# Performance work log

Hardware: AMD Instinct MI355X
Metric: run time of the kernel (lower is better)

Reference implementation:

```python
import jax, jax.numpy as jnp
import numpy as np

N_NODES = 50000
N_EDGES = 800000
IN_CH, HID_CH, OUT_CH = 128, 256, 128


def setup_inputs() -> dict:
    key = jax.random.key(0)
    k1, k2, k3, k4 = jax.random.split(key, 4)
    x = jax.random.normal(k1, (N_NODES, IN_CH), dtype=jnp.float32)
    edge_index = jax.random.randint(k2, (2, N_EDGES), 0, N_NODES, dtype=jnp.int32)
    # Glorot-ish scaled weights
    W1 = jax.random.normal(k3, (IN_CH, HID_CH), dtype=jnp.float32) * (1.0 / np.sqrt(IN_CH))
    b1 = jnp.zeros((HID_CH,), dtype=jnp.float32)
    W2 = jax.random.normal(k4, (HID_CH, OUT_CH), dtype=jnp.float32) * (1.0 / np.sqrt(HID_CH))
    b2 = jnpp = jnp.zeros((OUT_CH,), dtype=jnp.float32)
    return {"x": x, "edge_index": edge_index, "W1": W1, "b1": b1, "W2": W2, "b2": b2}


def _gcn_conv(x, W, b, src, dst, num_nodes):
    """PyG GCNConv: add self-loops, symmetric deg^-1/2 norm, linear, scatter-add."""
    h = x @ W  # [N, out] dense transform first (as in GCNConv)
    # in-degree including self-loops (edge weights = 1)
    deg = jax.ops.segment_sum(jnp.ones_like(dst, dtype=h.dtype), dst, num_segments=num_nodes)
    deg = deg + 1.0  # self-loop contribution
    dinv = jnp.where(deg > 0, jax.lax.rsqrt(deg), 0.0)
    # neighbor messages: norm_e * h[src_e], scatter-added to dst
    norm = dinv[src] * dinv[dst]                      # [E]
    msg = h[src] * norm[:, None]                      # [E, out] gather
    agg = jax.ops.segment_sum(msg, dst, num_segments=num_nodes)  # scatter-add
    # self-loop messages: dinv[i]^2 * h[i]
    agg = agg + h * (dinv * dinv)[:, None]
    return agg + b


def reference(x, edge_index, W1, b1, W2, b2):
    src, dst = edge_index[0], edge_index[1]
    n = x.shape[0]
    h = jax.nn.relu(_gcn_conv(x, W1, b1, src, dst, n))
    return _gcn_conv(h, W2, b2, src, dst, n)
```

## Files before the change

### kernel.cpp

```cpp
#include <hip/hip_runtime.h>

#define N_NODES 50000
#define N_EDGES 800000
#define IN_CH 128
#define HID_CH 256
#define OUT_CH 128
#define BUCKET 64

#define N_XCD 8
#define NODES_PER_XCD 6250

using half8 = __attribute__((ext_vector_type(8))) _Float16;
using f32x4 = __attribute__((ext_vector_type(4))) float;


#define FILL_CHUNKS 3125
#define FILL_BLOCKS (FILL_CHUNKS * N_XCD)
#define CVT_BLOCKS 3125
#define WT1_BLOCKS 256
#define WT2_BLOCKS 128

__global__ __launch_bounds__(256) void prep_kernel(const int* __restrict__ src,
                                                   const int* __restrict__ dst,
                                                   int* __restrict__ cnt,
                                                   unsigned short* __restrict__ bucket,
                                                   const float* __restrict__ x,
                                                   _Float16* __restrict__ x16,
                                                   const float* __restrict__ W1,
                                                   _Float16* __restrict__ W1T,
                                                   const float* __restrict__ W2,
                                                   _Float16* __restrict__ W2T) {
    int b = blockIdx.x, t = threadIdx.x;
    if (b < FILL_BLOCKS) {
        int g = b & 7;
        int chunk = b >> 3;
        int i = chunk * 256 + t;
        if (i < N_EDGES) {
            int d = dst[i];
            int lo = g * NODES_PER_XCD;
            if (d >= lo && d < lo + NODES_PER_XCD) {
                int s = src[i];
                int p = atomicAdd(&cnt[d], 1);
                if (p < BUCKET) bucket[(size_t)d * BUCKET + p] = (unsigned short)s;
            }
        }
    } else if (b < FILL_BLOCKS + CVT_BLOCKS) {
        int i = (b - FILL_BLOCKS) * 256 + t;
        float4 v0 = ((const float4*)x)[i * 2];
        float4 v1 = ((const float4*)x)[i * 2 + 1];
        half8 o = {(_Float16)v0.x, (_Float16)v0.y, (_Float16)v0.z, (_Float16)v0.w,
                   (_Float16)v1.x, (_Float16)v1.y, (_Float16)v1.z, (_Float16)v1.w};
        ((half8*)x16)[i] = o;
    } else if (b < FILL_BLOCKS + CVT_BLOCKS + WT1_BLOCKS) {
        int n = b - FILL_BLOCKS - CVT_BLOCKS;
        if (t < IN_CH) W1T[(size_t)n * IN_CH + t] = (_Float16)W1[(size_t)t * HID_CH + n];
    } else {
        int n = b - FILL_BLOCKS - CVT_BLOCKS - WT1_BLOCKS;
        if (t < HID_CH) W2T[(size_t)n * HID_CH + t] = (_Float16)W2[(size_t)t * OUT_CH + n];
    }
}


template <bool OUT16>
__global__ __launch_bounds__(256) void agg16_kernel(const _Float16* __restrict__ h16,
                                                    const int* __restrict__ cnt,
                                                    const unsigned short* __restrict__ bucket,
                                                    const float* __restrict__ bias,
                                                    void* __restrict__ outp) {
    int t = blockIdx.x * 256 + threadIdx.x;
    int v = t >> 4;
    int sub = t & 15;
    int deg = min(cnt[v], BUCKET);
    float dv = rsqrtf((float)cnt[v] + 1.0f);
    half8 hv = ((const half8*)(h16 + (size_t)v * 128))[sub];
    float acc[8];
#pragma unroll
    for (int i = 0; i < 8; i++) acc[i] = (float)hv[i] * dv * dv;

    const unsigned short* bk = bucket + (size_t)v * BUCKET;
    for (int base = 0; base < deg; base += 16) {
        int idx = base + sub;
        int a = 0;
        float c = 0.f;
        if (idx < deg) {
            a = bk[idx];
            c = rsqrtf((float)cnt[a] + 1.0f) * dv;
        }
        int len = min(deg - base, 16);
        int j = 0;
        for (; j + 8 <= len; j += 8) {
            int   s0 = __shfl(a, j + 0, 16); float w0 = __shfl(c, j + 0, 16);
            int   s1 = __shfl(a, j + 1, 16); float w1 = __shfl(c, j + 1, 16);
            int   s2 = __shfl(a, j + 2, 16); float w2 = __shfl(c, j + 2, 16);
            int   s3 = __shfl(a, j + 3, 16); float w3 = __shfl(c, j + 3, 16);
            int   s4 = __shfl(a, j + 4, 16); float w4 = __shfl(c, j + 4, 16);
            int   s5 = __shfl(a, j + 5, 16); float w5 = __shfl(c, j + 5, 16);
            int   s6 = __shfl(a, j + 6, 16); float w6 = __shfl(c, j + 6, 16);
            int   s7 = __shfl(a, j + 7, 16); float w7 = __shfl(c, j + 7, 16);
            half8 x0 = ((const half8*)(h16 + (size_t)s0 * 128))[sub];
            half8 x1 = ((const half8*)(h16 + (size_t)s1 * 128))[sub];
            half8 x2 = ((const half8*)(h16 + (size_t)s2 * 128))[sub];
            half8 x3 = ((const half8*)(h16 + (size_t)s3 * 128))[sub];
            half8 x4 = ((const half8*)(h16 + (size_t)s4 * 128))[sub];
            half8 x5 = ((const half8*)(h16 + (size_t)s5 * 128))[sub];
            half8 x6 = ((const half8*)(h16 + (size_t)s6 * 128))[sub];
            half8 x7 = ((const half8*)(h16 + (size_t)s7 * 128))[sub];
#pragma unroll
            for (int i = 0; i < 8; i++) acc[i] += w0 * (float)x0[i];
#pragma unroll
            for (int i = 0; i < 8; i++) acc[i] += w1 * (float)x1[i];
#pragma unroll
            for (int i = 0; i < 8; i++) acc[i] += w2 * (float)x2[i];
#pragma unroll
            for (int i = 0; i < 8; i++) acc[i] += w3 * (float)x3[i];
#pragma unroll
            for (int i = 0; i < 8; i++) acc[i] += w4 * (float)x4[i];
#pragma unroll
            for (int i = 0; i < 8; i++) acc[i] += w5 * (float)x5[i];
#pragma unroll
            for (int i = 0; i < 8; i++) acc[i] += w6 * (float)x6[i];
#pragma unroll
            for (int i = 0; i < 8; i++) acc[i] += w7 * (float)x7[i];
        }
        for (; j + 4 <= len; j += 4) {
            int   s0 = __shfl(a, j + 0, 16); float w0 = __shfl(c, j + 0, 16);
            int   s1 = __shfl(a, j + 1, 16); float w1 = __shfl(c, j + 1, 16);
            int   s2 = __shfl(a, j + 2, 16); float w2 = __shfl(c, j + 2, 16);
            int   s3 = __shfl(a, j + 3, 16); float w3 = __shfl(c, j + 3, 16);
            half8 x0 = ((const half8*)(h16 + (size_t)s0 * 128))[sub];
            half8 x1 = ((const half8*)(h16 + (size_t)s1 * 128))[sub];
            half8 x2 = ((const half8*)(h16 + (size_t)s2 * 128))[sub];
            half8 x3 = ((const half8*)(h16 + (size_t)s3 * 128))[sub];
#pragma unroll
            for (int i = 0; i < 8; i++) acc[i] += w0 * (float)x0[i];
#pragma unroll
            for (int i = 0; i < 8; i++) acc[i] += w1 * (float)x1[i];
#pragma unroll
            for (int i = 0; i < 8; i++) acc[i] += w2 * (float)x2[i];
#pragma unroll
            for (int i = 0; i < 8; i++) acc[i] += w3 * (float)x3[i];
        }
        for (; j < len; j++) {
            int   s = __shfl(a, j, 16);
            float w = __shfl(c, j, 16);
            half8 xv = ((const half8*)(h16 + (size_t)s * 128))[sub];
#pragma unroll
            for (int i = 0; i < 8; i++) acc[i] += w * (float)xv[i];
        }
    }

    if (OUT16) {
        half8 o;
#pragma unroll
        for (int i = 0; i < 8; i++) o[i] = (_Float16)acc[i];
        ((half8*)outp)[(size_t)v * 16 + sub] = o;
    } else {
        const float4* bp = (const float4*)bias;
        float4 b0 = bp[sub * 2], b1v = bp[sub * 2 + 1];
        float4 o0 = make_float4(acc[0] + b0.x, acc[1] + b0.y, acc[2] + b0.z, acc[3] + b0.w);
        float4 o1 = make_float4(acc[4] + b1v.x, acc[5] + b1v.y, acc[6] + b1v.z, acc[7] + b1v.w);
        float4* op = (float4*)outp;
        op[(size_t)v * 32 + sub * 2] = o0;
        op[(size_t)v * 32 + sub * 2 + 1] = o1;
    }
}


__global__ __launch_bounds__(256) void fused_mlp_kernel(const _Float16* __restrict__ A,
                                                        const _Float16* __restrict__ W1T,
                                                        const float* __restrict__ b1,
                                                        const _Float16* __restrict__ W2T,
                                                        _Float16* __restrict__ T2, int M) {
    const int LDH = 264;
    const int LDA = 136;
    const int LDB = 40;
    __shared__ __align__(16) _Float16 h1s[64 * LDH];
    __shared__ __align__(16) _Float16 As[64 * LDA];
    __shared__ __align__(16) _Float16 Bs[128 * LDB];

    int tid = threadIdx.x;
    int wave = tid >> 6, lane = tid & 63;
    int quad = lane >> 4, l16 = lane & 15;
    int wm = wave >> 1, wn = wave & 1;
    int bm = blockIdx.x * 64;

    for (int q = tid; q < 64 * 16; q += 256) {
        int row = q >> 4, seg = q & 15;
        int gr = bm + row;
        float4 v = make_float4(0.f, 0.f, 0.f, 0.f);
        if (gr < M) v = *(const float4*)(A + (size_t)gr * IN_CH + seg * 8);
        *(float4*)(As + row * LDA + seg * 8) = v;
    }

    for (int nh = 0; nh < 2; nh++) {
        f32x4 acc[2][4] = {};
        for (int k0 = 0; k0 < IN_CH; k0 += 32) {
            for (int q = tid; q < 512; q += 256) {
                int row = q >> 2, seg = q & 3;
                float4 v = *(const float4*)(W1T + (size_t)(nh * 128 + row) * IN_CH + k0 + seg * 8);
                *(float4*)(Bs + row * LDB + seg * 8) = v;
            }
            __syncthreads();
            half8 af[2], bf[4];
#pragma unroll
            for (int mt = 0; mt < 2; mt++)
                af[mt] = *(const half8*)(As + (wm * 32 + mt * 16 + l16) * LDA + k0 + quad * 8);
#pragma unroll
            for (int nt = 0; nt < 4; nt++)
                bf[nt] = *(const half8*)(Bs + (wn * 64 + nt * 16 + l16) * LDB + quad * 8);
#pragma unroll
            for (int mt = 0; mt < 2; mt++)
#pragma unroll
                for (int nt = 0; nt < 4; nt++)
                    acc[mt][nt] = __builtin_amdgcn_mfma_f32_16x16x32_f16(af[mt], bf[nt], acc[mt][nt], 0, 0, 0);
            __syncthreads();
        }
#pragma unroll
        for (int mt = 0; mt < 2; mt++)
#pragma unroll
            for (int nt = 0; nt < 4; nt++)
#pragma unroll
                for (int r = 0; r < 4; r++) {
                    int ml = wm * 32 + mt * 16 + quad * 4 + r;
                    int nl = wn * 64 + nt * 16 + l16;
                    float v = acc[mt][nt][r] + b1[nh * 128 + nl];
                    h1s[ml * LDH + nh * 128 + nl] = (_Float16)fmaxf(v, 0.f);
                }
    }

    f32x4 acc2[2][4] = {};
    for (int k0 = 0; k0 < HID_CH; k0 += 32) {
        for (int q = tid; q < 512; q += 256) {
            int row = q >> 2, seg = q & 3;
            float4 v = *(const float4*)(W2T + (size_t)row * HID_CH + k0 + seg * 8);
            *(float4*)(Bs + row * LDB + seg * 8) = v;
        }
        __syncthreads();
        half8 af[2], bf[4];
#pragma unroll
        for (int mt = 0; mt < 2; mt++)
            af[mt] = *(const half8*)(h1s + (wm * 32 + mt * 16 + l16) * LDH + k0 + quad * 8);
#pragma unroll
        for (int nt = 0; nt < 4; nt++)
            bf[nt] = *(const half8*)(Bs + (wn * 64 + nt * 16 + l16) * LDB + quad * 8);
#pragma unroll
        for (int mt = 0; mt < 2; mt++)
#pragma unroll
            for (int nt = 0; nt < 4; nt++)
                acc2[mt][nt] = __builtin_amdgcn_mfma_f32_16x16x32_f16(af[mt], bf[nt], acc2[mt][nt], 0, 0, 0);
        __syncthreads();
    }

    _Float16* Cs = As;
#pragma unroll
    for (int mt = 0; mt < 2; mt++)
#pragma unroll
        for (int nt = 0; nt < 4; nt++)
#pragma unroll
            for (int r = 0; r < 4; r++) {
                int ml = wm * 32 + mt * 16 + quad * 4 + r;
                int nl = wn * 64 + nt * 16 + l16;
                Cs[ml * LDA + nl] = (_Float16)acc2[mt][nt][r];
            }
    __syncthreads();
    for (int q = tid; q < 64 * 16; q += 256) {
        int row = q >> 4, seg = q & 15;
        int gr = bm + row;
        if (gr < M)
            *(float4*)(T2 + (size_t)gr * OUT_CH + seg * 8) = *(const float4*)(Cs + row * LDA + seg * 8);
    }
}


extern "C" void kernel_launch(void* const* d_in, const int* in_sizes, int n_in,
                              void* d_out, int out_size, void* d_ws, size_t ws_size,
                              hipStream_t stream) {
    const float* x  = (const float*)d_in[0];
    const int*   ei = (const int*)d_in[1];
    const int*   src = ei;
    const int*   dst = ei + N_EDGES;
    const float* W1 = (const float*)d_in[2];
    const float* b1 = (const float*)d_in[3];
    const float* W2 = (const float*)d_in[4];
    const float* b2 = (const float*)d_in[5];
    float* out = (float*)d_out;

    char* w = (char*)d_ws;
    auto alloc = [&](size_t bytes) -> void* {
        void* p = (void*)w;
        w += (bytes + 255) & ~(size_t)255;
        return p;
    };
    int*            cnt    = (int*)alloc((size_t)N_NODES * 4);
    unsigned short* bucket = (unsigned short*)alloc((size_t)N_NODES * BUCKET * 2);
    _Float16*       x16    = (_Float16*)alloc((size_t)N_NODES * IN_CH * 2);
    _Float16*       a1     = (_Float16*)alloc((size_t)N_NODES * IN_CH * 2);
    _Float16*       t2     = (_Float16*)alloc((size_t)N_NODES * OUT_CH * 2);
    _Float16*       W1T    = (_Float16*)alloc((size_t)IN_CH * HID_CH * 2);
    _Float16*       W2T    = (_Float16*)alloc((size_t)HID_CH * OUT_CH * 2);

    hipMemsetAsync(cnt, 0, (size_t)N_NODES * 4, stream);

    prep_kernel<<<FILL_BLOCKS + CVT_BLOCKS + WT1_BLOCKS + WT2_BLOCKS, 256, 0, stream>>>(
        src, dst, cnt, bucket, x, x16, W1, W1T, W2, W2T);

    agg16_kernel<true><<<N_NODES * 16 / 256, 256, 0, stream>>>(x16, cnt, bucket, nullptr, a1);
    fused_mlp_kernel<<<(N_NODES + 63) / 64, 256, 0, stream>>>(a1, W1T, b1, W2T, t2, N_NODES);
    agg16_kernel<false><<<N_NODES * 16 / 256, 256, 0, stream>>>(t2, cnt, bucket, b2, out);
}
```

Baseline: 216.2 us.

## Replace global-atomic CSR fill with two-pass LDS binning by destination block

Edge bucketing becomes two passes. The first kernel builds a per-block LDS histogram over 128-node bins, reserves space with one global atomic per bin, and writes packed (src, local dst) entries into bin buffers. A second kernel per bin counts and fills per-node buckets with LDS atomics and writes cnt directly. This removes the 8x redundant scan of the edge list and the per-edge global atomics on cnt, at the cost of an extra launch and a fixed bin capacity that can drop edges if a bin overflows.

```diff
diff --git a/kernel.cpp b/kernel.cpp
--- a/kernel.cpp
+++ b/kernel.cpp
@@ -7,57 +7,100 @@
 #define OUT_CH 128
 #define BUCKET 64
 
-#define N_XCD 8
-#define NODES_PER_XCD 6250
-
 using half8 = __attribute__((ext_vector_type(8))) _Float16;
 using f32x4 = __attribute__((ext_vector_type(4))) float;
 
 
-#define FILL_CHUNKS 3125
-#define FILL_BLOCKS (FILL_CHUNKS * N_XCD)
+#define NB 391
+#define NPB 128
+#define BIN_CAP 2432
+#define A_CHUNK 2048
+#define A_BLOCKS 391
+
 #define CVT_BLOCKS 3125
 #define WT1_BLOCKS 256
 #define WT2_BLOCKS 128
 
-__global__ __launch_bounds__(256) void prep_kernel(const int* __restrict__ src,
-                                                   const int* __restrict__ dst,
-                                                   int* __restrict__ cnt,
-                                                   unsigned short* __restrict__ bucket,
-                                                   const float* __restrict__ x,
-                                                   _Float16* __restrict__ x16,
-                                                   const float* __restrict__ W1,
-                                                   _Float16* __restrict__ W1T,
-                                                   const float* __restrict__ W2,
-                                                   _Float16* __restrict__ W2T) {
+__global__ __launch_bounds__(256) void prepA_kernel(const int* __restrict__ src,
+                                                    const int* __restrict__ dst,
+                                                    int* __restrict__ bin_fill,
+                                                    unsigned int* __restrict__ binbuf,
+                                                    const float* __restrict__ x,
+                                                    _Float16* __restrict__ x16,
+                                                    const float* __restrict__ W1,
+                                                    _Float16* __restrict__ W1T,
+                                                    const float* __restrict__ W2,
+                                                    _Float16* __restrict__ W2T) {
+    __shared__ int hist[NB];
+    __shared__ int lbase[NB];
+    __shared__ int cur[NB];
     int b = blockIdx.x, t = threadIdx.x;
-    if (b < FILL_BLOCKS) {
-        int g = b & 7;
-        int chunk = b >> 3;
-        int i = chunk * 256 + t;
-        if (i < N_EDGES) {
-            int d = dst[i];
-            int lo = g * NODES_PER_XCD;
-            if (d >= lo && d < lo + NODES_PER_XCD) {
+    if (b < A_BLOCKS) {
+        for (int i = t; i < NB; i += 256) {
+            hist[i] = 0;
+            cur[i] = 0;
+        }
+        __syncthreads();
+        int e0 = b * A_CHUNK;
+        int d[8];
+#pragma unroll
+        for (int k = 0; k < 8; k++) {
+            int i = e0 + k * 256 + t;
+            d[k] = (i < N_EDGES) ? dst[i] : -1;
+            if (d[k] >= 0) atomicAdd(&hist[d[k] >> 7], 1);
+        }
+        __syncthreads();
+        for (int i = t; i < NB; i += 256)
+            if (hist[i]) lbase[i] = atomicAdd(&bin_fill[i], hist[i]);
+        __syncthreads();
+#pragma unroll
+        for (int k = 0; k < 8; k++) {
+            int i = e0 + k * 256 + t;
+            if (d[k] >= 0) {
+                int bin = d[k] >> 7;
                 int s = src[i];
-                int p = atomicAdd(&cnt[d], 1);
-                if (p < BUCKET) bucket[(size_t)d * BUCKET + p] = (unsigned short)s;
+                int o = atomicAdd(&cur[bin], 1);
+                int pos = lbase[bin] + o;
+                if (pos < BIN_CAP)
+                    binbuf[(size_t)bin * BIN_CAP + pos] =
+                        (unsigned)s | ((unsigned)(d[k] & (NPB - 1)) << 16);
             }
         }
-    } else if (b < FILL_BLOCKS + CVT_BLOCKS) {
-        int i = (b - FILL_BLOCKS) * 256 + t;
+    } else if (b < A_BLOCKS + CVT_BLOCKS) {
+        int i = (b - A_BLOCKS) * 256 + t;
         float4 v0 = ((const float4*)x)[i * 2];
         float4 v1 = ((const float4*)x)[i * 2 + 1];
         half8 o = {(_Float16)v0.x, (_Float16)v0.y, (_Float16)v0.z, (_Float16)v0.w,
                    (_Float16)v1.x, (_Float16)v1.y, (_Float16)v1.z, (_Float16)v1.w};
         ((half8*)x16)[i] = o;
-    } else if (b < FILL_BLOCKS + CVT_BLOCKS + WT1_BLOCKS) {
-        int n = b - FILL_BLOCKS - CVT_BLOCKS;
+    } else if (b < A_BLOCKS + CVT_BLOCKS + WT1_BLOCKS) {
+        int n = b - A_BLOCKS - CVT_BLOCKS;
         if (t < IN_CH) W1T[(size_t)n * IN_CH + t] = (_Float16)W1[(size_t)t * HID_CH + n];
     } else {
-        int n = b - FILL_BLOCKS - CVT_BLOCKS - WT1_BLOCKS;
+        int n = b - A_BLOCKS - CVT_BLOCKS - WT1_BLOCKS;
         if (t < HID_CH) W2T[(size_t)n * HID_CH + t] = (_Float16)W2[(size_t)t * OUT_CH + n];
     }
+}
+
+__global__ __launch_bounds__(256) void prepB_kernel(const int* __restrict__ bin_fill,
+                                                    const unsigned int* __restrict__ binbuf,
+                                                    int* __restrict__ cnt,
+                                                    unsigned short* __restrict__ bucket) {
+    __shared__ int lcnt[NPB];
+    int bin = blockIdx.x, t = threadIdx.x;
+    if (t < NPB) lcnt[t] = 0;
+    __syncthreads();
+    int n = min(bin_fill[bin], BIN_CAP);
+    for (int i = t; i < n; i += 256) {
+        unsigned e = binbuf[(size_t)bin * BIN_CAP + i];
+        int dl = e >> 16;
+        int s = e & 0xFFFF;
+        int p = atomicAdd(&lcnt[dl], 1);
+        if (p < BUCKET) bucket[((size_t)(bin * NPB + dl)) * BUCKET + p] = (unsigned short)s;
+    }
+    __syncthreads();
+    int v = bin * NPB + t;
+    if (t < NPB && v < N_NODES) cnt[v] = lcnt[t];
 }
 
 
@@ -291,18 +334,21 @@
         w += (bytes + 255) & ~(size_t)255;
         return p;
     };
-    int*            cnt    = (int*)alloc((size_t)N_NODES * 4);
-    unsigned short* bucket = (unsigned short*)alloc((size_t)N_NODES * BUCKET * 2);
-    _Float16*       x16    = (_Float16*)alloc((size_t)N_NODES * IN_CH * 2);
-    _Float16*       a1     = (_Float16*)alloc((size_t)N_NODES * IN_CH * 2);
-    _Float16*       t2     = (_Float16*)alloc((size_t)N_NODES * OUT_CH * 2);
-    _Float16*       W1T    = (_Float16*)alloc((size_t)IN_CH * HID_CH * 2);
-    _Float16*       W2T    = (_Float16*)alloc((size_t)HID_CH * OUT_CH * 2);
-
-    hipMemsetAsync(cnt, 0, (size_t)N_NODES * 4, stream);
-
-    prep_kernel<<<FILL_BLOCKS + CVT_BLOCKS + WT1_BLOCKS + WT2_BLOCKS, 256, 0, stream>>>(
-        src, dst, cnt, bucket, x, x16, W1, W1T, W2, W2T);
+    int*            cnt     = (int*)alloc((size_t)N_NODES * 4);
+    unsigned short* bucket  = (unsigned short*)alloc((size_t)N_NODES * BUCKET * 2);
+    _Float16*       x16     = (_Float16*)alloc((size_t)N_NODES * IN_CH * 2);
+    _Float16*       a1      = (_Float16*)alloc((size_t)N_NODES * IN_CH * 2);
+    _Float16*       t2      = (_Float16*)alloc((size_t)N_NODES * OUT_CH * 2);
+    _Float16*       W1T     = (_Float16*)alloc((size_t)IN_CH * HID_CH * 2);
+    _Float16*       W2T     = (_Float16*)alloc((size_t)HID_CH * OUT_CH * 2);
+    int*            bin_fill = (int*)alloc((size_t)NB * 4);
+    unsigned int*   binbuf   = (unsigned int*)alloc((size_t)NB * BIN_CAP * 4);
+
+    hipMemsetAsync(bin_fill, 0, (size_t)NB * 4, stream);
+
+    prepA_kernel<<<A_BLOCKS + CVT_BLOCKS + WT1_BLOCKS + WT2_BLOCKS, 256, 0, stream>>>(
+        src, dst, bin_fill, binbuf, x, x16, W1, W1T, W2, W2T);
+    prepB_kernel<<<NB, 256, 0, stream>>>(bin_fill, binbuf, cnt, bucket);
 
     agg16_kernel<true><<<N_NODES * 16 / 256, 256, 0, stream>>>(x16, cnt, bucket, nullptr, a1);
     fused_mlp_kernel<<<(N_NODES + 63) / 64, 256, 0, stream>>>(a1, W1T, b1, W2T, t2, N_NODES);
```

Result: faster. 205.0 us (-5.2%).
